# Kernel optimization log

Hardware: AMD Instinct MI355X
Metric: run time of the kernel (lower is better)

Reference implementation:

```python
import jax, jax.numpy as jnp
import numpy as np

N = 50000       # num_node
E = 800000      # num edges (avg degree 32)
F_IN, F_HID, F_OUT = 128, 128, 64


def setup_inputs() -> dict:
    key = jax.random.key(0)
    ks = jax.random.split(key, 8)
    x = jax.random.normal(ks[0], (N, F_IN), dtype=jnp.float32)
    edge_index = jax.random.randint(ks[1], (2, E), 0, N, dtype=jnp.int64)
    edge_weight = jax.random.uniform(ks[2], (E,), dtype=jnp.float32)
    s1 = 1.0 / np.sqrt(F_IN)
    s2 = 1.0 / np.sqrt(F_HID)
    W1 = jax.random.normal(ks[3], (F_HID, F_IN), dtype=jnp.float32) * s1
    b1 = jnp.zeros((F_HID,), dtype=jnp.float32)
    W2 = jax.random.normal(ks[4], (F_HID, F_HID), dtype=jnp.float32) * s2
    b2 = jnp.zeros((F_HID,), dtype=jnp.float32)
    W3 = jax.random.normal(ks[5], (F_OUT, F_HID), dtype=jnp.float32) * s2
    b3 = jnp.zeros((F_OUT,), dtype=jnp.float32)
    return {"x": x, "edge_index": edge_index, "edge_weight": edge_weight,
            "W1": W1, "b1": b1, "W2": W2, "b2": b2, "W3": W3, "b3": b3}


def _gcn_norm(edge_index, edge_weight, num_nodes):
    # PyG gcn_norm: add self-loops (weight 1), symmetric D^-1/2 (A+I) D^-1/2
    loop = jnp.arange(num_nodes, dtype=edge_index.dtype)
    row = jnp.concatenate([edge_index[0], loop])  # source
    col = jnp.concatenate([edge_index[1], loop])  # target (aggregation index)
    ew = jnp.concatenate([edge_weight, jnp.ones((num_nodes,), edge_weight.dtype)])
    deg = jax.ops.segment_sum(ew, col, num_segments=num_nodes)
    deg_safe = jnp.where(deg > 0, deg, 1.0)
    dinv = jnp.where(deg > 0, jax.lax.rsqrt(deg_safe), 0.0)
    norm = dinv[row] * ew * dinv[col]  # [E+N]
    return row, col, norm


def reference(x, edge_index, edge_weight, W1, b1, W2, b2, W3, b3):
    num_nodes = x.shape[0]
    row, col, norm = _gcn_norm(edge_index, edge_weight, num_nodes)
    h = x
    for W, b in ((W1, b1), (W2, b2), (W3, b3)):
        m = h @ W.T                                   # [N, d_out]
        msg = m[row] * norm[:, None]                  # gather + scale, [E+N, d_out]
        agg = jax.ops.segment_sum(msg, col, num_segments=num_nodes)
        h = jax.nn.relu(agg + b)                      # GCNConv bias then ReLU
    return h.reshape(-1)                              # torch.flatten
```

## Files before the change

### kernel.cpp

```cpp
#include <hip/hip_runtime.h>
#include <hip/hip_fp16.h>


#define K_DIM 128
#define SORT_ITEMS 4096

typedef unsigned long long u64;
typedef unsigned int u32;

using half8   = __attribute__((ext_vector_type(8))) _Float16;
using floatx4 = __attribute__((ext_vector_type(4))) float;


__global__ void build_hist(const int* __restrict__ row, const int* __restrict__ col,
                           const float* __restrict__ ew, u64* __restrict__ el,
                           u32* __restrict__ ghist, int E, int N, int nb,
                           const float* __restrict__ W1, const float* __restrict__ W2,
                           const float* __restrict__ W3, __half* __restrict__ Wh,
                           int nw1, int nw2, int nw3) {
    const int b = blockIdx.x;
    if (b >= nb) {
        const int i = (b - nb) * 256 + threadIdx.x;
        const int tot = nw1 + nw2 + nw3;
        if (i < tot) {
            float v = (i < nw1) ? W1[i] : (i < nw1 + nw2 ? W2[i - nw1] : W3[i - nw1 - nw2]);
            Wh[i] = __float2half_rn(v);
        }
        return;
    }
    __shared__ u32 bin[256];
    bin[threadIdx.x] = 0;
    __syncthreads();
    const int total = E + N;
    const int base = b * SORT_ITEMS;
    const int end = min(base + SORT_ITEMS, total);
    for (int i = base + threadIdx.x; i < end; i += 256) {
        u64 e;
        if (i < E) {
            e = ((u64)(u32)col[i] << 48) | ((u64)(u32)row[i] << 32)
              | (u64)__float_as_uint(ew[i]);
        } else {
            int v = i - E;
            e = ((u64)(u32)v << 48) | ((u64)(u32)v << 32)
              | (u64)__float_as_uint(1.0f);
        }
        el[i] = e;
        atomicAdd(&bin[(u32)(e >> 56)], 1u);
    }
    __syncthreads();
    ghist[(size_t)threadIdx.x * nb + b] = bin[threadIdx.x];
}

__global__ void digit_sum(const u32* __restrict__ ghist, u32* __restrict__ dsum, int nb) {
    __shared__ u32 s[256];
    const int d = blockIdx.x;
    u32 acc = 0;
    for (int i = threadIdx.x; i < nb; i += 256) acc += ghist[(size_t)d * nb + i];
    s[threadIdx.x] = acc;
    __syncthreads();
    for (int off = 128; off > 0; off >>= 1) {
        if (threadIdx.x < off) s[threadIdx.x] += s[threadIdx.x + off];
        __syncthreads();
    }
    if (threadIdx.x == 0) dsum[d] = s[0];
}

__global__ void digit_scan(u32* __restrict__ ghist, const u32* __restrict__ dsum,
                           u32* __restrict__ dbase, int nb) {
    __shared__ u32 ds[256];
    __shared__ u32 s[256];
    const int d = blockIdx.x, t = threadIdx.x;
    ds[t] = dsum[t];
    __syncthreads();
    for (int off = 1; off < 256; off <<= 1) {
        u32 u = (t >= off) ? ds[t - off] : 0;
        __syncthreads();
        ds[t] += u;
        __syncthreads();
    }
    u32 carry = (d == 0) ? 0u : ds[d - 1];
    if (t == 0) dbase[d] = carry;
    if (d == 255 && t == 0) dbase[256] = ds[255];
    for (int base = 0; base < nb; base += 256) {
        const int i = base + t;
        const u32 v = (i < nb) ? ghist[(size_t)d * nb + i] : 0;
        s[t] = v;
        __syncthreads();
        for (int off = 1; off < 256; off <<= 1) {
            u32 u = (t >= off) ? s[t - off] : 0;
            __syncthreads();
            s[t] += u;
            __syncthreads();
        }
        if (i < nb) ghist[(size_t)d * nb + i] = carry + s[t] - v;
        carry += s[255];
        __syncthreads();
    }
}

__global__ __launch_bounds__(256) void p1_gemm(const u64* __restrict__ el,
                                               const u32* __restrict__ ghist,
                                               u64* __restrict__ out, int total, int nb,
                                               const float* __restrict__ x,
                                               const __half* __restrict__ Wh,
                                               __half* __restrict__ C, int n) {
    __shared__ u32 gbase[256];
    __shared__ u32 lbase[256];
    __shared__ u32 lcur[256];
    __shared__ u64 buf[SORT_ITEMS];
    if ((int)blockIdx.x >= nb) {
        const int gb = blockIdx.x - nb;
        const int wave = threadIdx.x >> 6;
        const int lane = threadIdx.x & 63;
        const int quad = lane >> 4;
        const int l16  = lane & 15;
        const int row0 = gb * 64 + wave * 16;

        int arow = row0 + l16;
        if (arow > n - 1) arow = n - 1;

        floatx4 acc[8] = {};
#pragma unroll
        for (int kc = 0; kc < 4; ++kc) {
            const int kof = kc * 32 + quad * 8;
            const float* ap = x + (size_t)arow * K_DIM + kof;
            float4 f0 = *(const float4*)ap;
            float4 f1 = *(const float4*)(ap + 4);
            half8 af;
            af[0] = (_Float16)f0.x; af[1] = (_Float16)f0.y;
            af[2] = (_Float16)f0.z; af[3] = (_Float16)f0.w;
            af[4] = (_Float16)f1.x; af[5] = (_Float16)f1.y;
            af[6] = (_Float16)f1.z; af[7] = (_Float16)f1.w;
#pragma unroll
            for (int ct = 0; ct < 8; ++ct) {
                half8 bf = *(const half8*)(Wh + (size_t)(ct * 16 + l16) * K_DIM + kof);
                acc[ct] = __builtin_amdgcn_mfma_f32_16x16x32_f16(af, bf, acc[ct], 0, 0, 0);
            }
        }
        int grow[4];
        bool okr[4];
#pragma unroll
        for (int r = 0; r < 4; ++r) {
            grow[r] = row0 + quad * 4 + r;
            okr[r] = grow[r] < n;
        }
#pragma unroll
        for (int ct = 0; ct < 8; ++ct) {
            const int colb = ct * 16 + l16;
#pragma unroll
            for (int r = 0; r < 4; ++r)
                if (okr[r])
                    C[(size_t)grow[r] * 128 + colb] = __float2half_rn(acc[ct][r]);
        }
        return;
    }
    const int t = threadIdx.x;
    gbase[t] = ghist[(size_t)t * nb + blockIdx.x];
    lcur[t] = 0;
    __syncthreads();
    const int base = blockIdx.x * SORT_ITEMS;
    const int end = min(base + SORT_ITEMS, total);
    const int cnt = end - base;

    u64 it[16];
    bool ok[16];
#pragma unroll
    for (int j = 0; j < 16; ++j) {
        const int i = base + t + j * 256;
        ok[j] = i < end;
        it[j] = ok[j] ? el[i] : 0;
        if (ok[j]) atomicAdd(&lcur[(u32)(it[j] >> 56)], 1u);
    }
    __syncthreads();
    const u32 v = lcur[t];
    lbase[t] = v;
    __syncthreads();
    for (int off = 1; off < 256; off <<= 1) {
        u32 u = (t >= off) ? lbase[t - off] : 0;
        __syncthreads();
        lbase[t] += u;
        __syncthreads();
    }
    const u32 excl = lbase[t] - v;
    __syncthreads();
    lbase[t] = excl;
    lcur[t] = excl;
    __syncthreads();
#pragma unroll
    for (int j = 0; j < 16; ++j) {
        if (ok[j]) {
            const u32 d = (u32)(it[j] >> 56);
            const u32 p = atomicAdd(&lcur[d], 1u);
            buf[p] = it[j];
        }
    }
    __syncthreads();
    for (int i = t; i < cnt; i += 256) {
        const u64 e = buf[i];
        const u32 d = (u32)(e >> 56);
        out[gbase[d] + i - lbase[d]] = e;
    }
}

__global__ __launch_bounds__(1024) void p2_gemm(
        const u64* __restrict__ in, u64* __restrict__ out,
        const u32* __restrict__ dbase,
        int* __restrict__ offs, float* __restrict__ dinv, int n, int ngroups,
        const float* __restrict__ x, const __half* __restrict__ Wh,
        __half* __restrict__ C, int rowoff) {
    if ((int)blockIdx.x < ngroups) {
        const int t = threadIdx.x;
        const int q = t >> 8;
        const int b = t & 255;
        const int base = (int)dbase[blockIdx.x];
        const int size = (int)dbase[blockIdx.x + 1] - base;
        __shared__ u32 hist[4][256];
        __shared__ u32 cur[4][256];
        __shared__ u32 s[256];
        __shared__ float wsum[4][256];
        hist[q][b] = 0;
        wsum[q][b] = 0.f;
        __syncthreads();
        for (int i = t; i < size; i += 1024)
            atomicAdd(&hist[q][(u32)(in[base + i] >> 48) & 0xFFu], 1u);
        __syncthreads();
        u32 v = 0;
        if (t < 256) {
            v = hist[0][b] + hist[1][b] + hist[2][b] + hist[3][b];
            s[b] = v;
        }
        __syncthreads();
        for (int off = 1; off < 256; off <<= 1) {
            u32 u = (t < 256 && b >= off) ? s[b - off] : 0;
            __syncthreads();
            if (t < 256) s[b] += u;
            __syncthreads();
        }
        u32 mystart = 0;
        if (t < 256) {
            mystart = (u32)base + s[b] - v;
            u32 c = mystart;
            cur[0][b] = c; c += hist[0][b];
            cur[1][b] = c; c += hist[1][b];
            cur[2][b] = c; c += hist[2][b];
            cur[3][b] = c;
        }
        __syncthreads();
        for (int i = t; i < size; i += 1024) {
            u64 e = in[base + i];
            u32 lo = (u32)(e >> 48) & 0xFFu;
            u32 p = atomicAdd(&cur[q][lo], 1u);
            out[p] = e;
            atomicAdd(&wsum[q][lo], __uint_as_float((u32)(e & 0xFFFFFFFFu)));
        }
        __syncthreads();
        const int node = blockIdx.x * 256 + b;
        if (t < 256 && node < n && v > 0) {
            offs[node] = (int)mystart;
            dinv[node] = rsqrtf(wsum[0][b] + wsum[1][b] + wsum[2][b] + wsum[3][b]);
            if (node == n - 1) offs[n] = (int)(mystart + v);
        }
    } else {
        const int gb = blockIdx.x - ngroups;
        const int wave = threadIdx.x >> 6;
        const int lane = threadIdx.x & 63;
        const int quad = lane >> 4;
        const int l16  = lane & 15;
        const int row0 = rowoff + gb * 256 + wave * 16;

        int arow = row0 + l16;
        if (arow > n - 1) arow = n - 1;

        floatx4 acc[8] = {};
#pragma unroll
        for (int kc = 0; kc < 4; ++kc) {
            const int kof = kc * 32 + quad * 8;
            const float* ap = x + (size_t)arow * K_DIM + kof;
            float4 f0 = *(const float4*)ap;
            float4 f1 = *(const float4*)(ap + 4);
            half8 af;
            af[0] = (_Float16)f0.x; af[1] = (_Float16)f0.y;
            af[2] = (_Float16)f0.z; af[3] = (_Float16)f0.w;
            af[4] = (_Float16)f1.x; af[5] = (_Float16)f1.y;
            af[6] = (_Float16)f1.z; af[7] = (_Float16)f1.w;
#pragma unroll
            for (int ct = 0; ct < 8; ++ct) {
                half8 bf = *(const half8*)(Wh + (size_t)(ct * 16 + l16) * K_DIM + kof);
                acc[ct] = __builtin_amdgcn_mfma_f32_16x16x32_f16(af, bf, acc[ct], 0, 0, 0);
            }
        }
        int grow[4];
        bool ok[4];
#pragma unroll
        for (int r = 0; r < 4; ++r) {
            grow[r] = row0 + quad * 4 + r;
            ok[r] = grow[r] < n;
        }
#pragma unroll
        for (int ct = 0; ct < 8; ++ct) {
            const int colb = ct * 16 + l16;
#pragma unroll
            for (int r = 0; r < 4; ++r)
                if (ok[r])
                    C[(size_t)grow[r] * 128 + colb] = __float2half_rn(acc[ct][r]);
        }
    }
}


template <int BN>
__global__ __launch_bounds__(256) void mfma_gemm(const __half* __restrict__ Ain,
                                                 const __half* __restrict__ Wh,
                                                 __half* __restrict__ C, int nrows) {
    constexpr int NT = BN / 16;
    const int wave = threadIdx.x >> 6;
    const int lane = threadIdx.x & 63;
    const int quad = lane >> 4;
    const int l16  = lane & 15;
    const int row0 = blockIdx.x * 64 + wave * 16;

    int arow = row0 + l16;
    if (arow > nrows - 1) arow = nrows - 1;

    floatx4 acc[NT] = {};

#pragma unroll
    for (int kc = 0; kc < 4; ++kc) {
        const int kof = kc * 32 + quad * 8;
        half8 af = *(const half8*)(Ain + (size_t)arow * K_DIM + kof);
#pragma unroll
        for (int ct = 0; ct < NT; ++ct) {
            half8 bf = *(const half8*)(Wh + (size_t)(ct * 16 + l16) * K_DIM + kof);
            acc[ct] = __builtin_amdgcn_mfma_f32_16x16x32_f16(af, bf, acc[ct], 0, 0, 0);
        }
    }

    int grow[4];
    bool ok[4];
#pragma unroll
    for (int r = 0; r < 4; ++r) {
        grow[r] = row0 + quad * 4 + r;
        ok[r] = grow[r] < nrows;
    }
#pragma unroll
    for (int ct = 0; ct < NT; ++ct) {
        const int colb = ct * 16 + l16;
#pragma unroll
        for (int r = 0; r < 4; ++r)
            if (ok[r])
                C[(size_t)grow[r] * BN + colb] = __float2half_rn(acc[ct][r]);
    }
}


template <int D, typename OUT>
__global__ __launch_bounds__(256) void agg_kernel(
    const __half* __restrict__ m, const int* __restrict__ offs,
    const int2* __restrict__ csr, const float* __restrict__ dinv,
    const float* __restrict__ bias, OUT* __restrict__ out, int n) {
    const int wid = threadIdx.x >> 6;
    const int lane = threadIdx.x & 63;
    const int node = (blockIdx.x << 2) + wid;
    if (node >= n) return;
    const int beg = offs[node];
    const int end = offs[node + 1];
    const int cnt = end - beg;
    const half8* mrow = (const half8*)m;

    const int2 ev = csr[beg + min(lane, cnt - 1)];
    const int   sv = ev.y & 0xFFFF;
    const float ds = dinv[sv];
    const float wv = (lane < cnt) ? __int_as_float(ev.x) * ds : 0.f;
    const int nr = min(cnt, 64);

    float acc[8] = {0.f, 0.f, 0.f, 0.f, 0.f, 0.f, 0.f, 0.f};

    if constexpr (D == 128) {
        const int quad = lane >> 4;
        const int l16  = lane & 15;
        const int rem = nr & 15;
        if (rem) {
            float w0 = __shfl(wv, quad),      w1 = __shfl(wv, 4 + quad);
            float w2 = __shfl(wv, 8 + quad),  w3 = __shfl(wv, 12 + quad);
            int   s0 = __shfl(sv, quad),      s1 = __shfl(sv, 4 + quad);
            int   s2 = __shfl(sv, 8 + quad),  s3 = __shfl(sv, 12 + quad);
            w0 = (quad      < rem) ? w0 : 0.f;
            w1 = (4 + quad  < rem) ? w1 : 0.f;
            w2 = (8 + quad  < rem) ? w2 : 0.f;
            w3 = (12 + quad < rem) ? w3 : 0.f;
            half8 h0 = mrow[(size_t)s0 * 16 + l16];
            half8 h1 = mrow[(size_t)s1 * 16 + l16];
            half8 h2 = mrow[(size_t)s2 * 16 + l16];
            half8 h3 = mrow[(size_t)s3 * 16 + l16];
#pragma unroll
            for (int i = 0; i < 8; ++i) {
                acc[i] = fmaf(w0, (float)h0[i], acc[i]);
                acc[i] = fmaf(w1, (float)h1[i], acc[i]);
                acc[i] = fmaf(w2, (float)h2[i], acc[i]);
                acc[i] = fmaf(w3, (float)h3[i], acc[i]);
            }
        }
        for (int k = rem; k < nr; k += 16) {
            float w0 = __shfl(wv, k + quad),      w1 = __shfl(wv, k + 4 + quad);
            float w2 = __shfl(wv, k + 8 + quad),  w3 = __shfl(wv, k + 12 + quad);
            int   s0 = __shfl(sv, k + quad),      s1 = __shfl(sv, k + 4 + quad);
            int   s2 = __shfl(sv, k + 8 + quad),  s3 = __shfl(sv, k + 12 + quad);
            half8 h0 = mrow[(size_t)s0 * 16 + l16];
            half8 h1 = mrow[(size_t)s1 * 16 + l16];
            half8 h2 = mrow[(size_t)s2 * 16 + l16];
            half8 h3 = mrow[(size_t)s3 * 16 + l16];
#pragma unroll
            for (int i = 0; i < 8; ++i) {
                acc[i] = fmaf(w0, (float)h0[i], acc[i]);
                acc[i] = fmaf(w1, (float)h1[i], acc[i]);
                acc[i] = fmaf(w2, (float)h2[i], acc[i]);
                acc[i] = fmaf(w3, (float)h3[i], acc[i]);
            }
        }
        for (int k = beg + 64 + quad; k < end; k += 4) {
            const int2 e0 = csr[k];
            const int  s0 = e0.y & 0xFFFF;
            const float w0 = __int_as_float(e0.x) * dinv[s0];
            half8 hv = mrow[(size_t)s0 * 16 + l16];
#pragma unroll
            for (int i = 0; i < 8; ++i)
                acc[i] = fmaf(w0, (float)hv[i], acc[i]);
        }
#pragma unroll
        for (int i = 0; i < 8; ++i) {
            acc[i] += __shfl_xor(acc[i], 16);
            acc[i] += __shfl_xor(acc[i], 32);
        }
        if (quad == 0) {
            const float dv = dinv[node];
            const float4 b0 = *(const float4*)(bias + l16 * 8);
            const float4 b1 = *(const float4*)(bias + l16 * 8 + 4);
            const float bb[8] = {b0.x, b0.y, b0.z, b0.w, b1.x, b1.y, b1.z, b1.w};
            half8 ho;
#pragma unroll
            for (int i = 0; i < 8; ++i)
                ho[i] = (_Float16)fmaxf(acc[i] * dv + bb[i], 0.f);
            *(half8*)((__half*)out + (size_t)node * 128 + l16 * 8) = ho;
        }
    } else {
        const int oct = lane >> 3;
        const int l8  = lane & 7;
        const int rem = nr & 31;
        if (rem) {
            float w0 = __shfl(wv, oct),       w1 = __shfl(wv, 8 + oct);
            float w2 = __shfl(wv, 16 + oct),  w3 = __shfl(wv, 24 + oct);
            int   s0 = __shfl(sv, oct),       s1 = __shfl(sv, 8 + oct);
            int   s2 = __shfl(sv, 16 + oct),  s3 = __shfl(sv, 24 + oct);
            w0 = (oct      < rem) ? w0 : 0.f;
            w1 = (8 + oct  < rem) ? w1 : 0.f;
            w2 = (16 + oct < rem) ? w2 : 0.f;
            w3 = (24 + oct < rem) ? w3 : 0.f;
            half8 h0 = mrow[(size_t)s0 * 8 + l8];
            half8 h1 = mrow[(size_t)s1 * 8 + l8];
            half8 h2 = mrow[(size_t)s2 * 8 + l8];
            half8 h3 = mrow[(size_t)s3 * 8 + l8];
#pragma unroll
            for (int i = 0; i < 8; ++i) {
                acc[i] = fmaf(w0, (float)h0[i], acc[i]);
                acc[i] = fmaf(w1, (float)h1[i], acc[i]);
                acc[i] = fmaf(w2, (float)h2[i], acc[i]);
                acc[i] = fmaf(w3, (float)h3[i], acc[i]);
            }
        }
        for (int k = rem; k < nr; k += 32) {
            float w0 = __shfl(wv, k + oct),       w1 = __shfl(wv, k + 8 + oct);
            float w2 = __shfl(wv, k + 16 + oct),  w3 = __shfl(wv, k + 24 + oct);
            int   s0 = __shfl(sv, k + oct),       s1 = __shfl(sv, k + 8 + oct);
            int   s2 = __shfl(sv, k + 16 + oct),  s3 = __shfl(sv, k + 24 + oct);
            half8 h0 = mrow[(size_t)s0 * 8 + l8];
            half8 h1 = mrow[(size_t)s1 * 8 + l8];
            half8 h2 = mrow[(size_t)s2 * 8 + l8];
            half8 h3 = mrow[(size_t)s3 * 8 + l8];
#pragma unroll
            for (int i = 0; i < 8; ++i) {
                acc[i] = fmaf(w0, (float)h0[i], acc[i]);
                acc[i] = fmaf(w1, (float)h1[i], acc[i]);
                acc[i] = fmaf(w2, (float)h2[i], acc[i]);
                acc[i] = fmaf(w3, (float)h3[i], acc[i]);
            }
        }
        for (int k = beg + 64 + oct; k < end; k += 8) {
            const int2 e0 = csr[k];
            const int  s0 = e0.y & 0xFFFF;
            const float w0 = __int_as_float(e0.x) * dinv[s0];
            half8 hv = mrow[(size_t)s0 * 8 + l8];
#pragma unroll
            for (int i = 0; i < 8; ++i)
                acc[i] = fmaf(w0, (float)hv[i], acc[i]);
        }
#pragma unroll
        for (int i = 0; i < 8; ++i) {
            acc[i] += __shfl_xor(acc[i], 8);
            acc[i] += __shfl_xor(acc[i], 16);
            acc[i] += __shfl_xor(acc[i], 32);
        }
        if (oct == 0) {
            const float dv = dinv[node];
            const float4 b0 = *(const float4*)(bias + l8 * 8);
            const float4 b1 = *(const float4*)(bias + l8 * 8 + 4);
            float4 v0, v1;
            v0.x = fmaxf(acc[0] * dv + b0.x, 0.f);
            v0.y = fmaxf(acc[1] * dv + b0.y, 0.f);
            v0.z = fmaxf(acc[2] * dv + b0.z, 0.f);
            v0.w = fmaxf(acc[3] * dv + b0.w, 0.f);
            v1.x = fmaxf(acc[4] * dv + b1.x, 0.f);
            v1.y = fmaxf(acc[5] * dv + b1.y, 0.f);
            v1.z = fmaxf(acc[6] * dv + b1.z, 0.f);
            v1.w = fmaxf(acc[7] * dv + b1.w, 0.f);
            float* op = (float*)out + (size_t)node * 64 + l8 * 8;
            *(float4*)op = v0;
            *(float4*)(op + 4) = v1;
        }
    }
}


extern "C" void kernel_launch(void* const* d_in, const int* in_sizes, int n_in,
                              void* d_out, int out_size, void* d_ws, size_t ws_size,
                              hipStream_t stream) {
    const float* x  = (const float*)d_in[0];
    const int*   ei = (const int*)d_in[1];
    const float* ew = (const float*)d_in[2];
    const float* W1 = (const float*)d_in[3];
    const float* b1 = (const float*)d_in[4];
    const float* W2 = (const float*)d_in[5];
    const float* b2 = (const float*)d_in[6];
    const float* W3 = (const float*)d_in[7];
    const float* b3 = (const float*)d_in[8];
    float* out = (float*)d_out;

    const int N = in_sizes[0] / K_DIM;
    const int E = in_sizes[2];
    const int* row = ei;
    const int* col = ei + E;

    const int total = E + N;
    const int nb = (total + SORT_ITEMS - 1) / SORT_ITEMS;
    const int ngroups = (N + 255) >> 8;
    const int NW1 = 128 * 128, NW2 = 128 * 128, NW3 = 64 * 128;
    const int nwb = (NW1 + NW2 + NW3 + 255) / 256;

    u64* elA      = (u64*)d_ws;
    u64* elB      = elA + total;
    __half* m_buf = (__half*)(elB + total);
    __half* h_buf = m_buf + (size_t)N * K_DIM;
    __half* Wh    = h_buf + (size_t)N * K_DIM;
    u32* ghist    = (u32*)(Wh + NW1 + NW2 + NW3);
    u32* dsum     = ghist + (size_t)256 * nb;
    u32* dbase    = dsum + 256;
    int* offs     = (int*)(dbase + 257);
    float* dinv   = (float*)(offs + N + 1);

    build_hist<<<nb + nwb, 256, 0, stream>>>(row, col, ew, elA, ghist, E, N, nb,
                                             W1, W2, W3, Wh, NW1, NW2, NW3);
    digit_sum<<<256, 256, 0, stream>>>(ghist, dsum, nb);
    digit_scan<<<256, 256, 0, stream>>>(ghist, dsum, dbase, nb);

    const int g1blocks = 392;
    const int g1rows = g1blocks * 64;
    p1_gemm<<<nb + g1blocks, 256, 0, stream>>>(elA, ghist, elB, total, nb,
                                               x, Wh, m_buf, N);

    const int g2blocks = (N - g1rows + 255) / 256;
    p2_gemm<<<ngroups + g2blocks, 1024, 0, stream>>>(
        elB, elA, dbase, offs, dinv, N, ngroups, x, Wh, m_buf, g1rows);

    const int gemm_blocks = (N + 63) / 64;
    const int agg_blocks = (N + 3) / 4;
    const int2* csr = (const int2*)elA;

    agg_kernel<128, __half><<<agg_blocks, 256, 0, stream>>>(m_buf, offs, csr, dinv, b1, h_buf, N);
    mfma_gemm<128><<<gemm_blocks, 256, 0, stream>>>(h_buf, Wh + NW1, m_buf, N);
    agg_kernel<128, __half><<<agg_blocks, 256, 0, stream>>>(m_buf, offs, csr, dinv, b2, h_buf, N);
    mfma_gemm<64><<<gemm_blocks, 256, 0, stream>>>(h_buf, Wh + NW1 + NW2, m_buf, N);
    agg_kernel<64, float><<<agg_blocks, 256, 0, stream>>>(m_buf, offs, csr, dinv, b3, out, N);
}
```

Measured before the change: 268.9 us.

## Split aggregation feature columns across two block halves to double edge parallelism

The aggregation kernel now launches twice as many blocks. Each half of the grid handles one half of the feature columns for every node, so a wave gathers narrower row slices but covers more edges per step (8 edges at a time for D=128, 16 for D=64). The aim is more independent memory requests in flight during the latency-bound neighbor gather. In exchange, the CSR entries, dinv values and offsets are read twice, and each gathered row segment is smaller.

Result: slower. 316.6 us (+17.7%).

```diff
diff --git a/kernel.cpp b/kernel.cpp
--- a/kernel.cpp
+++ b/kernel.cpp
@@ -358,9 +358,12 @@
     const __half* __restrict__ m, const int* __restrict__ offs,
     const int2* __restrict__ csr, const float* __restrict__ dinv,
     const float* __restrict__ bias, OUT* __restrict__ out, int n) {
+    const int nbh = (n + 3) >> 2;
+    const int half = ((int)blockIdx.x >= nbh) ? 1 : 0;
+    const int blk = blockIdx.x - half * nbh;
     const int wid = threadIdx.x >> 6;
     const int lane = threadIdx.x & 63;
-    const int node = (blockIdx.x << 2) + wid;
+    const int node = (blk << 2) + wid;
     if (node >= n) return;
     const int beg = offs[node];
     const int end = offs[node + 1];
@@ -376,75 +379,9 @@
     float acc[8] = {0.f, 0.f, 0.f, 0.f, 0.f, 0.f, 0.f, 0.f};
 
     if constexpr (D == 128) {
-        const int quad = lane >> 4;
-        const int l16  = lane & 15;
-        const int rem = nr & 15;
-        if (rem) {
-            float w0 = __shfl(wv, quad),      w1 = __shfl(wv, 4 + quad);
-            float w2 = __shfl(wv, 8 + quad),  w3 = __shfl(wv, 12 + quad);
-            int   s0 = __shfl(sv, quad),      s1 = __shfl(sv, 4 + quad);
-            int   s2 = __shfl(sv, 8 + quad),  s3 = __shfl(sv, 12 + quad);
-            w0 = (quad      < rem) ? w0 : 0.f;
-            w1 = (4 + quad  < rem) ? w1 : 0.f;
-            w2 = (8 + quad  < rem) ? w2 : 0.f;
-            w3 = (12 + quad < rem) ? w3 : 0.f;
-            half8 h0 = mrow[(size_t)s0 * 16 + l16];
-            half8 h1 = mrow[(size_t)s1 * 16 + l16];
-            half8 h2 = mrow[(size_t)s2 * 16 + l16];
-            half8 h3 = mrow[(size_t)s3 * 16 + l16];
-#pragma unroll
-            for (int i = 0; i < 8; ++i) {
-                acc[i] = fmaf(w0, (float)h0[i], acc[i]);
-                acc[i] = fmaf(w1, (float)h1[i], acc[i]);
-                acc[i] = fmaf(w2, (float)h2[i], acc[i]);
-                acc[i] = fmaf(w3, (float)h3[i], acc[i]);
-            }
-        }
-        for (int k = rem; k < nr; k += 16) {
-            float w0 = __shfl(wv, k + quad),      w1 = __shfl(wv, k + 4 + quad);
-            float w2 = __shfl(wv, k + 8 + quad),  w3 = __shfl(wv, k + 12 + quad);
-            int   s0 = __shfl(sv, k + quad),      s1 = __shfl(sv, k + 4 + quad);
-            int   s2 = __shfl(sv, k + 8 + quad),  s3 = __shfl(sv, k + 12 + quad);
-            half8 h0 = mrow[(size_t)s0 * 16 + l16];
-            half8 h1 = mrow[(size_t)s1 * 16 + l16];
-            half8 h2 = mrow[(size_t)s2 * 16 + l16];
-            half8 h3 = mrow[(size_t)s3 * 16 + l16];
-#pragma unroll
-            for (int i = 0; i < 8; ++i) {
-                acc[i] = fmaf(w0, (float)h0[i], acc[i]);
-                acc[i] = fmaf(w1, (float)h1[i], acc[i]);
-                acc[i] = fmaf(w2, (float)h2[i], acc[i]);
-                acc[i] = fmaf(w3, (float)h3[i], acc[i]);
-            }
-        }
-        for (int k = beg + 64 + quad; k < end; k += 4) {
-            const int2 e0 = csr[k];
-            const int  s0 = e0.y & 0xFFFF;
-            const float w0 = __int_as_float(e0.x) * dinv[s0];
-            half8 hv = mrow[(size_t)s0 * 16 + l16];
-#pragma unroll
-            for (int i = 0; i < 8; ++i)
-                acc[i] = fmaf(w0, (float)hv[i], acc[i]);
-        }
-#pragma unroll
-        for (int i = 0; i < 8; ++i) {
-            acc[i] += __shfl_xor(acc[i], 16);
-            acc[i] += __shfl_xor(acc[i], 32);
-        }
-        if (quad == 0) {
-            const float dv = dinv[node];
-            const float4 b0 = *(const float4*)(bias + l16 * 8);
-            const float4 b1 = *(const float4*)(bias + l16 * 8 + 4);
-            const float bb[8] = {b0.x, b0.y, b0.z, b0.w, b1.x, b1.y, b1.z, b1.w};
-            half8 ho;
-#pragma unroll
-            for (int i = 0; i < 8; ++i)
-                ho[i] = (_Float16)fmaxf(acc[i] * dv + bb[i], 0.f);
-            *(half8*)((__half*)out + (size_t)node * 128 + l16 * 8) = ho;
-        }
-    } else {
         const int oct = lane >> 3;
         const int l8  = lane & 7;
+        const int hb  = half * 8;
         const int rem = nr & 31;
         if (rem) {
             float w0 = __shfl(wv, oct),       w1 = __shfl(wv, 8 + oct);
@@ -455,10 +392,10 @@
             w1 = (8 + oct  < rem) ? w1 : 0.f;
             w2 = (16 + oct < rem) ? w2 : 0.f;
             w3 = (24 + oct < rem) ? w3 : 0.f;
-            half8 h0 = mrow[(size_t)s0 * 8 + l8];
-            half8 h1 = mrow[(size_t)s1 * 8 + l8];
-            half8 h2 = mrow[(size_t)s2 * 8 + l8];
-            half8 h3 = mrow[(size_t)s3 * 8 + l8];
+            half8 h0 = mrow[(size_t)s0 * 16 + hb + l8];
+            half8 h1 = mrow[(size_t)s1 * 16 + hb + l8];
+            half8 h2 = mrow[(size_t)s2 * 16 + hb + l8];
+            half8 h3 = mrow[(size_t)s3 * 16 + hb + l8];
 #pragma unroll
             for (int i = 0; i < 8; ++i) {
                 acc[i] = fmaf(w0, (float)h0[i], acc[i]);
@@ -472,10 +409,10 @@
             float w2 = __shfl(wv, k + 16 + oct),  w3 = __shfl(wv, k + 24 + oct);
             int   s0 = __shfl(sv, k + oct),       s1 = __shfl(sv, k + 8 + oct);
             int   s2 = __shfl(sv, k + 16 + oct),  s3 = __shfl(sv, k + 24 + oct);
-            half8 h0 = mrow[(size_t)s0 * 8 + l8];
-            half8 h1 = mrow[(size_t)s1 * 8 + l8];
-            half8 h2 = mrow[(size_t)s2 * 8 + l8];
-            half8 h3 = mrow[(size_t)s3 * 8 + l8];
+            half8 h0 = mrow[(size_t)s0 * 16 + hb + l8];
+            half8 h1 = mrow[(size_t)s1 * 16 + hb + l8];
+            half8 h2 = mrow[(size_t)s2 * 16 + hb + l8];
+            half8 h3 = mrow[(size_t)s3 * 16 + hb + l8];
 #pragma unroll
             for (int i = 0; i < 8; ++i) {
                 acc[i] = fmaf(w0, (float)h0[i], acc[i]);
@@ -488,7 +425,7 @@
             const int2 e0 = csr[k];
             const int  s0 = e0.y & 0xFFFF;
             const float w0 = __int_as_float(e0.x) * dinv[s0];
-            half8 hv = mrow[(size_t)s0 * 8 + l8];
+            half8 hv = mrow[(size_t)s0 * 16 + hb + l8];
 #pragma unroll
             for (int i = 0; i < 8; ++i)
                 acc[i] = fmaf(w0, (float)hv[i], acc[i]);
@@ -501,8 +438,80 @@
         }
         if (oct == 0) {
             const float dv = dinv[node];
-            const float4 b0 = *(const float4*)(bias + l8 * 8);
-            const float4 b1 = *(const float4*)(bias + l8 * 8 + 4);
+            const float* bp = bias + half * 64 + l8 * 8;
+            const float4 b0 = *(const float4*)bp;
+            const float4 b1 = *(const float4*)(bp + 4);
+            const float bb[8] = {b0.x, b0.y, b0.z, b0.w, b1.x, b1.y, b1.z, b1.w};
+            half8 ho;
+#pragma unroll
+            for (int i = 0; i < 8; ++i)
+                ho[i] = (_Float16)fmaxf(acc[i] * dv + bb[i], 0.f);
+            *(half8*)((__half*)out + (size_t)node * 128 + half * 64 + l8 * 8) = ho;
+        }
+    } else {
+        const int grp = lane >> 2;
+        const int l4  = lane & 3;
+        const int hb  = half * 4;
+        const int rem = nr & 63;
+        if (rem) {
+            float w0 = __shfl(wv, grp),       w1 = __shfl(wv, 16 + grp);
+            float w2 = __shfl(wv, 32 + grp),  w3 = __shfl(wv, 48 + grp);
+            int   s0 = __shfl(sv, grp),       s1 = __shfl(sv, 16 + grp);
+            int   s2 = __shfl(sv, 32 + grp),  s3 = __shfl(sv, 48 + grp);
+            w0 = (grp      < rem) ? w0 : 0.f;
+            w1 = (16 + grp < rem) ? w1 : 0.f;
+            w2 = (32 + grp < rem) ? w2 : 0.f;
+            w3 = (48 + grp < rem) ? w3 : 0.f;
+            half8 h0 = mrow[(size_t)s0 * 8 + hb + l4];
+            half8 h1 = mrow[(size_t)s1 * 8 + hb + l4];
+            half8 h2 = mrow[(size_t)s2 * 8 + hb + l4];
+            half8 h3 = mrow[(size_t)s3 * 8 + hb + l4];
+#pragma unroll
+            for (int i = 0; i < 8; ++i) {
+                acc[i] = fmaf(w0, (float)h0[i], acc[i]);
+                acc[i] = fmaf(w1, (float)h1[i], acc[i]);
+                acc[i] = fmaf(w2, (float)h2[i], acc[i]);
+                acc[i] = fmaf(w3, (float)h3[i], acc[i]);
+            }
+        }
+        if (rem < nr) {
+            float w0 = __shfl(wv, grp),       w1 = __shfl(wv, 16 + grp);
+            float w2 = __shfl(wv, 32 + grp),  w3 = __shfl(wv, 48 + grp);
+            int   s0 = __shfl(sv, grp),       s1 = __shfl(sv, 16 + grp);
+            int   s2 = __shfl(sv, 32 + grp),  s3 = __shfl(sv, 48 + grp);
+            half8 h0 = mrow[(size_t)s0 * 8 + hb + l4];
+            half8 h1 = mrow[(size_t)s1 * 8 + hb + l4];
+            half8 h2 = mrow[(size_t)s2 * 8 + hb + l4];
+            half8 h3 = mrow[(size_t)s3 * 8 + hb + l4];
+#pragma unroll
+            for (int i = 0; i < 8; ++i) {
+                acc[i] = fmaf(w0, (float)h0[i], acc[i]);
+                acc[i] = fmaf(w1, (float)h1[i], acc[i]);
+                acc[i] = fmaf(w2, (float)h2[i], acc[i]);
+                acc[i] = fmaf(w3, (float)h3[i], acc[i]);
+            }
+        }
+        for (int k = beg + 64 + grp; k < end; k += 16) {
+            const int2 e0 = csr[k];
+            const int  s0 = e0.y & 0xFFFF;
+            const float w0 = __int_as_float(e0.x) * dinv[s0];
+            half8 hv = mrow[(size_t)s0 * 8 + hb + l4];
+#pragma unroll
+            for (int i = 0; i < 8; ++i)
+                acc[i] = fmaf(w0, (float)hv[i], acc[i]);
+        }
+#pragma unroll
+        for (int i = 0; i < 8; ++i) {
+            acc[i] += __shfl_xor(acc[i], 4);
+            acc[i] += __shfl_xor(acc[i], 8);
+            acc[i] += __shfl_xor(acc[i], 16);
+            acc[i] += __shfl_xor(acc[i], 32);
+        }
+        if (grp == 0) {
+            const float dv = dinv[node];
+            const float* bp = bias + half * 32 + l4 * 8;
+            const float4 b0 = *(const float4*)bp;
+            const float4 b1 = *(const float4*)(bp + 4);
             float4 v0, v1;
             v0.x = fmaxf(acc[0] * dv + b0.x, 0.f);
             v0.y = fmaxf(acc[1] * dv + b0.y, 0.f);
@@ -512,7 +521,7 @@
             v1.y = fmaxf(acc[5] * dv + b1.y, 0.f);
             v1.z = fmaxf(acc[6] * dv + b1.z, 0.f);
             v1.w = fmaxf(acc[7] * dv + b1.w, 0.f);
-            float* op = (float*)out + (size_t)node * 64 + l8 * 8;
+            float* op = (float*)out + (size_t)node * 64 + half * 32 + l4 * 8;
             *(float4*)op = v0;
             *(float4*)(op + 4) = v1;
         }
@@ -571,12 +580,12 @@
         elB, elA, dbase, offs, dinv, N, ngroups, x, Wh, m_buf, g1rows);
 
     const int gemm_blocks = (N + 63) / 64;
-    const int agg_blocks = (N + 3) / 4;
+    const int agg_blocks2 = 2 * ((N + 3) / 4);
     const int2* csr = (const int2*)elA;
 
-    agg_kernel<128, __half><<<agg_blocks, 256, 0, stream>>>(m_buf, offs, csr, dinv, b1, h_buf, N);
+    agg_kernel<128, __half><<<agg_blocks2, 256, 0, stream>>>(m_buf, offs, csr, dinv, b1, h_buf, N);
     mfma_gemm<128><<<gemm_blocks, 256, 0, stream>>>(h_buf, Wh + NW1, m_buf, N);
-    agg_kernel<128, __half><<<agg_blocks, 256, 0, stream>>>(m_buf, offs, csr, dinv, b2, h_buf, N);
+    agg_kernel<128, __half><<<agg_blocks2, 256, 0, stream>>>(m_buf, offs, csr, dinv, b2, h_buf, N);
     mfma_gemm<64><<<gemm_blocks, 256, 0, stream>>>(h_buf, Wh + NW1 + NW2, m_buf, N);
-    agg_kernel<64, float><<<agg_blocks, 256, 0, stream>>>(m_buf, offs, csr, dinv, b3, out, N);
-}
+    agg_kernel<64, float><<<agg_blocks2, 256, 0, stream>>>(m_buf, offs, csr, dinv, b3, out, N);
+}
```
